# Kernel tuning notes

Hardware: AMD Instinct MI355X
Metric: run time of the kernel (lower is better)

The kernel has to match this reference:

```python
import jax, jax.numpy as jnp
import numpy as np

# Module config (matches init_kwargs)
W_BIT = 2
PS_BIT = 8
IC = 256
OC = 256
K = 3
N_XBAR = 576
STRIDE = 1
PAD = 1
NUM_IC = min(IC, N_XBAR // (K * K))   # 64 input channels per crossbar array
GROUPS = IC // NUM_IC                 # 4 arrays (col_slide), ic divides evenly
QP_W = 2 ** W_BIT - 1                 # unsigned levels for nonneg pos/neg weights
QN_PS = -(2 ** (PS_BIT - 1))          # signed psum range
QP_PS = 2 ** (PS_BIT - 1) - 1


def lsq(v, s, qn, qp):
    """LSQ quantize-dequantize with straight-through rounding."""
    vs = jnp.clip(v / s, qn, qp)
    vbar = vs + jax.lax.stop_gradient(jnp.round(vs) - vs)
    return vbar * s


def conv2d(x, w):
    # x: [B, C, H, W], w: [O, C, k, k]
    return jax.lax.conv_general_dilated(
        x, w, window_strides=(STRIDE, STRIDE),
        padding=((PAD, PAD), (PAD, PAD)),
        dimension_numbers=('NCHW', 'OIHW', 'NCHW'))


def setup_inputs() -> dict:
    key = jax.random.key(0)
    k1, k2, k3, k4, k5 = jax.random.split(key, 5)
    x = jax.random.normal(k1, (16, IC, 56, 56), dtype=jnp.float32)
    weight = jax.random.normal(k2, (OC, IC, K, K), dtype=jnp.float32) * 0.05
    # positive LSQ step sizes, roughly 2*E|w|/sqrt(Qp) scale
    w_scale = jax.random.uniform(k3, (GROUPS,), dtype=jnp.float32) * 0.04 + 0.01
    ps_scale_p = jax.random.uniform(k4, (GROUPS,), dtype=jnp.float32) * 0.05 + 0.02
    ps_scale_n = jax.random.uniform(k5, (GROUPS,), dtype=jnp.float32) * 0.05 + 0.02
    return {"x": x, "weight": weight, "w_scale": w_scale,
            "ps_scale_p": ps_scale_p, "ps_scale_n": ps_scale_n}


def reference(x, weight, w_scale, ps_scale_p, ps_scale_n):
    B, _, H, W = x.shape
    # im2col tiling over input channels into GROUPS crossbar arrays
    xg = x.reshape(B, GROUPS, NUM_IC, H, W)                  # [B,G,cg,H,W]
    wg = weight.reshape(OC, GROUPS, NUM_IC, K, K)            # [O,G,cg,k,k]
    # pos / neg weight split, per-array LSQ weight quantization (shared quantizer)
    s_w = w_scale[:, None, None, None, None]                 # [G,1,1,1,1]
    wg_t = jnp.transpose(wg, (1, 0, 2, 3, 4))                # [G,O,cg,k,k]
    wq_p = lsq(jax.nn.relu(wg_t), s_w, 0, QP_W)
    wq_n = lsq(jax.nn.relu(-wg_t), s_w, 0, QP_W)
    xg_t = jnp.transpose(xg, (1, 0, 2, 3, 4))                # [G,B,cg,H,W]
    # per-array partial-sum convs (vmapped over arrays)
    vconv = jax.vmap(conv2d, in_axes=(0, 0))
    psum_p = vconv(xg_t, wq_p)                               # [G,B,O,h,w]
    psum_n = vconv(xg_t, wq_n)
    # per-array psum LSQ quantization ('Array' mode), then accumulate
    s_p = ps_scale_p[:, None, None, None, None]
    s_n = ps_scale_n[:, None, None, None, None]
    out_p = jnp.sum(lsq(psum_p, s_p, QN_PS, QP_PS), axis=0)  # [B,O,h,w]
    out_n = jnp.sum(lsq(psum_n, s_n, QN_PS, QP_PS), axis=0)
    return out_p - out_n
```

## Files before the change

kernel.cpp:

```cpp
#include <hip/hip_runtime.h>
#include <hip/hip_bf16.h>

typedef __attribute__((ext_vector_type(8))) short bf16x8_t;
typedef __attribute__((ext_vector_type(4))) float f32x4_t;

#define XP_BYTES 55115776u
#define WT_BYTES 4718592u

typedef __attribute__((address_space(1))) const unsigned int ga_u32_t;
typedef __attribute__((address_space(3))) unsigned int lds_u32_t;

__device__ __forceinline__ void g2l16(const void* g, void* l) {
  __builtin_amdgcn_global_load_lds((ga_u32_t*)g, (lds_u32_t*)l, 16, 0, 0);
}

__global__ __launch_bounds__(256) void prep_x(const float* __restrict__ x,
                                              __hip_bfloat16* __restrict__ xp) {
  __shared__ float ls[64 * 57];
  int blk = blockIdx.x;
  int g = blk / 896;
  int r = blk - g * 896;
  int b = r / 56;
  int h = r - b * 56;
  int tid = threadIdx.x;
  const float* src = x + (size_t)(b * 256 + g * 64) * 3136 + h * 56;
  for (int i = tid; i < 64 * 56; i += 256) {
    int c = i / 56, w = i - c * 56;
    ls[c * 57 + w] = src[(size_t)c * 3136 + w];
  }
  __syncthreads();
  __hip_bfloat16* dst = xp + ((size_t)((g * 16 + b) * 58 + h + 1) * 58 + 1) * 128;
  int wp = tid >> 7;
  int inner = tid & 127;
  int hl = inner >> 6, c = inner & 63;
  for (int w0 = 0; w0 < 56; w0 += 2) {
    int w = w0 + wp;
    float v = ls[c * 57 + w];
    __hip_bfloat16 hi = __float2bfloat16(v);
    __hip_bfloat16 val = hl ? __float2bfloat16(v - __bfloat162float(hi)) : hi;
    dst[(size_t)w * 128 + inner] = val;
  }
}

__global__ __launch_bounds__(256) void prep_w(const float* __restrict__ wgt,
                                              const float* __restrict__ wsc,
                                              __hip_bfloat16* __restrict__ wt) {
  int idx = blockIdx.x * 256 + threadIdx.x;
  if (idx >= 589824) return;
  int oc = idx / 2304;
  int r = idx - oc * 2304;
  int C = r / 9;
  int tap = r - C * 9;
  int g = C >> 6, c = C & 63;
  float s = wsc[g];
  float rv = wgt[idx] / s;
  float ip = rintf(fminf(fmaxf(rv, 0.f), 3.f));
  float iN = rintf(fminf(fmaxf(-rv, 0.f), 3.f));
  size_t base_p = (size_t)(g * 512 + oc) * 1152 + tap * 128 + c;
  size_t base_n = base_p + (size_t)256 * 1152;
  __hip_bfloat16 vp = __float2bfloat16(ip);
  __hip_bfloat16 vn = __float2bfloat16(iN);
  wt[base_p] = vp;
  wt[base_p + 64] = vp;
  wt[base_n] = vn;
  wt[base_n + 64] = vn;
}

#define MEMPIN asm volatile("" ::: "memory")
#define BAR __builtin_amdgcn_s_barrier()
#define VMCNT6 asm volatile("s_waitcnt vmcnt(6)" ::: "memory")
#define VMCNT0 asm volatile("s_waitcnt vmcnt(0)" ::: "memory")

__global__ __launch_bounds__(512, 2) void conv_mfma(
    const unsigned short* __restrict__ xp, const unsigned short* __restrict__ wt,
    const float* __restrict__ wsc, const float* __restrict__ psp,
    const float* __restrict__ psn, float* __restrict__ out) {
  __shared__ char AB[3][49152];

  const int bid = blockIdx.x;
  const int wg = (bid & 7) * 49 + (bid >> 3);
  const int mblk = wg;

  const int tid = threadIdx.x;
  const int wv = tid >> 6;
  const int l = tid & 63;
  const int wr = wv >> 2, wc = wv & 3;

  const int srow = tid >> 3;
  const unsigned cs16 = (unsigned)(((tid & 7) ^ (srow & 7)) << 4);
  unsigned apix0, apix1, bofs0, bofs1, bofs2, bofs3;
  {
    int m0 = mblk * 128 + srow;
    int b0 = m0 / 3136, hw0 = m0 - b0 * 3136, h0 = hw0 / 56, w0 = hw0 - h0 * 56;
    apix0 = (unsigned)((b0 * 3364 + h0 * 58 + w0) * 256) + cs16;
    int m1 = m0 + 64;
    int b1 = m1 / 3136, hw1 = m1 - b1 * 3136, h1 = hw1 / 56, w1 = hw1 - h1 * 56;
    apix1 = (unsigned)((b1 * 3364 + h1 * 58 + w1) * 256) + cs16;
    bofs0 = (unsigned)(srow * 2304) + cs16;
    bofs1 = bofs0 + 64u * 2304u;
    bofs2 = bofs0 + 128u * 2304u;
    bofs3 = bofs0 + 192u * 2304u;
  }

  const unsigned a_base = (unsigned)((wr * 64 + (l & 15)) * 128);
  const unsigned b_base = (unsigned)(16384 + (wc * 64 + (l & 15)) * 128);
  const unsigned sw0 = (unsigned)((((l >> 4) + 0) ^ (l & 7)) << 4);
  const unsigned sw1 = (unsigned)((((l >> 4) + 4) ^ (l & 7)) << 4);

  float w0s = wsc[0], w1s = wsc[1], w2s = wsc[2], w3s = wsc[3];
  float p0 = psp[0], p1 = psp[1], p2 = psp[2], p3 = psp[3];
  float n0 = psn[0], n1 = psn[1], n2 = psn[2], n3 = psn[3];

  f32x4_t acc[4][4], oacc[4][4];
  const f32x4_t fz = {0.f, 0.f, 0.f, 0.f};
#pragma unroll
  for (int i = 0; i < 4; ++i)
#pragma unroll
    for (int j = 0; j < 4; ++j) { acc[i][j] = fz; oacc[i][j] = fz; }

  const char* xg = (const char*)xp;
  const char* wgp = (const char*)wt;

#define STAGE_A(t2)                                                            \
  {                                                                            \
    const int tt = (t2);                                                       \
    const int g_ = tt / 36;                                                    \
    const int r_ = tt - g_ * 36;                                               \
    const int s18 = (r_ >= 18) ? (r_ - 18) : r_;                               \
    const int tap_ = s18 >> 1, hl_ = s18 & 1;                                  \
    const unsigned at_ = (unsigned)g_ * 13778944u +                            \
                         (unsigned)(((tap_ / 3) * 58 + (tap_ % 3)) * 256) +    \
                         (unsigned)(hl_ << 7);                                 \
    char* lA_ = &AB[tt % 3][0] + (wv << 10);                                   \
    g2l16(xg + apix0 + at_, lA_);                                              \
    g2l16(xg + apix1 + at_, lA_ + 8192);                                       \
  }

#define STAGE_B(t2)                                                            \
  {                                                                            \
    const int tt = (t2);                                                       \
    const int g_ = tt / 36;                                                    \
    const int r_ = tt - g_ * 36;                                               \
    const int sgn_ = (r_ >= 18) ? 1 : 0;                                       \
    const int s18 = r_ - (sgn_ ? 18 : 0);                                      \
    const int tap_ = s18 >> 1, hl_ = s18 & 1;                                  \
    const unsigned bt_ = (unsigned)((g_ * 2 + sgn_) * 589824) +                \
                         (unsigned)((tap_ * 2 + hl_) << 7);                    \
    char* lB_ = &AB[tt % 3][16384] + (wv << 10);                               \
    g2l16(wgp + bofs0 + bt_, lB_);                                             \
    g2l16(wgp + bofs1 + bt_, lB_ + 8192);                                      \
    g2l16(wgp + bofs2 + bt_, lB_ + 16384);                                     \
    g2l16(wgp + bofs3 + bt_, lB_ + 24576);                                     \
  }

#define PHASE_MMA                                                              \
  __builtin_amdgcn_s_setprio(1);                                               \
  _Pragma("unroll") for (int mi = 0; mi < 4; ++mi)                             \
      _Pragma("unroll") for (int ni = 0; ni < 4; ++ni)                         \
          acc[mi][ni] = __builtin_amdgcn_mfma_f32_16x16x32_bf16(               \
              af[mi], bf[ni], acc[mi][ni], 0, 0, 0);                           \
  __builtin_amdgcn_s_setprio(0);

  STAGE_A(0); STAGE_B(0); STAGE_A(1); STAGE_B(1);

  for (int t = 0; t < 144; ++t) {
    if (t == 143) { VMCNT0; } else { VMCNT6; }
    BAR;
    MEMPIN;
    const char* buf = &AB[t % 3][0];
    bf16x8_t af[4], bf[4];
#pragma unroll
    for (int mi = 0; mi < 4; ++mi)
      af[mi] = *(const bf16x8_t*)(buf + a_base + mi * 2048 + sw0);
#pragma unroll
    for (int ni = 0; ni < 4; ++ni)
      bf[ni] = *(const bf16x8_t*)(buf + b_base + ni * 2048 + sw0);
    MEMPIN;
    if (t + 2 < 144) { STAGE_A(t + 2); }
    PHASE_MMA;
#pragma unroll
    for (int mi = 0; mi < 4; ++mi)
      af[mi] = *(const bf16x8_t*)(buf + a_base + mi * 2048 + sw1);
#pragma unroll
    for (int ni = 0; ni < 4; ++ni)
      bf[ni] = *(const bf16x8_t*)(buf + b_base + ni * 2048 + sw1);
    MEMPIN;
    if (t + 2 < 144) { STAGE_B(t + 2); }
    PHASE_MMA;

    if ((t % 18) == 17) {
      int gg = t / 36;
      int sgn = (t / 18) & 1;
      float sw = (gg & 2) ? ((gg & 1) ? w3s : w2s) : ((gg & 1) ? w1s : w0s);
      float sp = (gg & 2) ? ((gg & 1) ? p3 : p2) : ((gg & 1) ? p1 : p0);
      float sn = (gg & 2) ? ((gg & 1) ? n3 : n2) : ((gg & 1) ? n1 : n0);
      float sq = sgn ? sn : sp;
      float rs = sw / sq;
      float sgnmul = sgn ? -1.f : 1.f;
#pragma unroll
      for (int mi = 0; mi < 4; ++mi)
#pragma unroll
        for (int ni = 0; ni < 4; ++ni)
#pragma unroll
          for (int j = 0; j < 4; ++j) {
            float v = acc[mi][ni][j] * rs;
            v = fminf(fmaxf(v, -128.f), 127.f);
            oacc[mi][ni][j] += sgnmul * rintf(v) * sq;
            acc[mi][ni][j] = 0.f;
          }
    }
  }

#pragma unroll
  for (int ni = 0; ni < 4; ++ni) {
    int oc = wc * 64 + ni * 16 + (l & 15);
#pragma unroll
    for (int mi = 0; mi < 4; ++mi) {
      int m0 = mblk * 128 + wr * 64 + mi * 16 + ((l >> 4) << 2);
#pragma unroll
      for (int j = 0; j < 4; ++j) {
        int m = m0 + j;
        int b = m / 3136;
        int hw = m - b * 3136;
        out[(size_t)((b << 8) + oc) * 3136 + hw] = oacc[mi][ni][j];
      }
    }
  }
#undef STAGE_A
#undef STAGE_B
#undef PHASE_MMA
}

__global__ __launch_bounds__(256) void naive_conv(
    const float* __restrict__ x, const float* __restrict__ wgt,
    const float* __restrict__ wsc, const float* __restrict__ psp,
    const float* __restrict__ psn, float* __restrict__ out) {
  int idx = blockIdx.x * 256 + threadIdx.x;
  if (idx >= 12845056) return;
  int b = idx / 802816;
  int r = idx - b * 802816;
  int oc = r / 3136;
  int hw = r - oc * 3136;
  int h = hw / 56, w = hw - (hw / 56) * 56;
  float o = 0.f;
  for (int g = 0; g < 4; ++g) {
    float sw = wsc[g];
    float inv = 1.f / sw;
    float pp = 0.f, pn = 0.f;
    for (int tap = 0; tap < 9; ++tap) {
      int y = h + tap / 3 - 1, xx = w + tap % 3 - 1;
      if (y < 0 || y > 55 || xx < 0 || xx > 55) continue;
      const float* xr = x + (size_t)(b * 256 + g * 64) * 3136 + y * 56 + xx;
      const float* wrr = wgt + (size_t)oc * 2304 + (size_t)(g * 64) * 9 + tap;
      for (int c = 0; c < 64; ++c) {
        float xv = xr[(size_t)c * 3136];
        float rv = wrr[c * 9] * inv;
        pp += xv * rintf(fminf(fmaxf(rv, 0.f), 3.f));
        pn += xv * rintf(fminf(fmaxf(-rv, 0.f), 3.f));
      }
    }
    float sp = psp[g], sn = psn[g];
    o += rintf(fminf(fmaxf(pp * (sw / sp), -128.f), 127.f)) * sp;
    o -= rintf(fminf(fmaxf(pn * (sw / sn), -128.f), 127.f)) * sn;
  }
  out[idx] = o;
}

extern "C" void kernel_launch(void* const* d_in, const int* in_sizes, int n_in,
                              void* d_out, int out_size, void* d_ws, size_t ws_size,
                              hipStream_t stream) {
  const float* x = (const float*)d_in[0];
  const float* wgt = (const float*)d_in[1];
  const float* wsc = (const float*)d_in[2];
  const float* psp = (const float*)d_in[3];
  const float* psn = (const float*)d_in[4];
  float* out = (float*)d_out;

  if (ws_size >= (size_t)XP_BYTES + (size_t)WT_BYTES) {
    unsigned short* xpw = (unsigned short*)d_ws;
    unsigned short* wtw = (unsigned short*)((char*)d_ws + XP_BYTES);
    hipMemsetAsync(d_ws, 0, XP_BYTES, stream);
    prep_x<<<3584, 256, 0, stream>>>(x, (__hip_bfloat16*)xpw);
    prep_w<<<2304, 256, 0, stream>>>(wgt, wsc, (__hip_bfloat16*)wtw);
    conv_mfma<<<392, 512, 0, stream>>>(xpw, wtw, wsc, psp, psn, out);
  } else {
    naive_conv<<<(12845056 + 255) / 256, 256, 0, stream>>>(x, wgt, wsc, psp, psn, out);
  }
}
```

Before: 293.1 us.

## Stage one input row strip per group in LDS and reuse it across all taps

The A operand is no longer restaged from global memory for every tap. Each block now covers output rows of a single image and loads the padded input strip for a whole channel group (rows plus halo) into LDS once. All nine taps then index it with shifted pixel offsets. The weight layout drops the duplicated channel halves, so each step streams a 32-channel weight tile. This cuts global and L2 traffic for activations. In exchange, the bulk strip load at each group boundary is not overlapped with compute, and the larger LDS footprint likely limits the kernel to one block per CU.

```diff
diff --git a/kernel.cpp b/kernel.cpp
--- a/kernel.cpp
+++ b/kernel.cpp
@@ -5,7 +5,7 @@
 typedef __attribute__((ext_vector_type(4))) float f32x4_t;
 
 #define XP_BYTES 55115776u
-#define WT_BYTES 4718592u
+#define WT_BYTES 2359296u
 
 typedef __attribute__((address_space(1))) const unsigned int ga_u32_t;
 typedef __attribute__((address_space(3))) unsigned int lds_u32_t;
@@ -56,56 +56,49 @@
   float rv = wgt[idx] / s;
   float ip = rintf(fminf(fmaxf(rv, 0.f), 3.f));
   float iN = rintf(fminf(fmaxf(-rv, 0.f), 3.f));
-  size_t base_p = (size_t)(g * 512 + oc) * 1152 + tap * 128 + c;
-  size_t base_n = base_p + (size_t)256 * 1152;
-  __hip_bfloat16 vp = __float2bfloat16(ip);
-  __hip_bfloat16 vn = __float2bfloat16(iN);
-  wt[base_p] = vp;
-  wt[base_p + 64] = vp;
-  wt[base_n] = vn;
-  wt[base_n + 64] = vn;
+  size_t base_p = (size_t)((g * 2 + 0) * 256 + oc) * 576 + tap * 64 + c;
+  size_t base_n = (size_t)((g * 2 + 1) * 256 + oc) * 576 + tap * 64 + c;
+  wt[base_p] = __float2bfloat16(ip);
+  wt[base_n] = __float2bfloat16(iN);
 }
 
 #define MEMPIN asm volatile("" ::: "memory")
 #define BAR __builtin_amdgcn_s_barrier()
-#define VMCNT6 asm volatile("s_waitcnt vmcnt(6)" ::: "memory")
+#define VMCNT2 asm volatile("s_waitcnt vmcnt(2)" ::: "memory")
 #define VMCNT0 asm volatile("s_waitcnt vmcnt(0)" ::: "memory")
 
 __global__ __launch_bounds__(512, 2) void conv_mfma(
     const unsigned short* __restrict__ xp, const unsigned short* __restrict__ wt,
     const float* __restrict__ wsc, const float* __restrict__ psp,
     const float* __restrict__ psn, float* __restrict__ out) {
-  __shared__ char AB[3][49152];
+  __shared__ char Astrip[89088];
+  __shared__ char Bbuf[3][16384];
 
   const int bid = blockIdx.x;
-  const int wg = (bid & 7) * 49 + (bid >> 3);
-  const int mblk = wg;
+  const int wg = (bid & 7) * 50 + (bid >> 3);
+  const int b = wg / 25;
+  const int tile = wg - b * 25;
+  int r0 = (tile * 128) / 56; if (r0 > 52) r0 = 52;
 
   const int tid = threadIdx.x;
   const int wv = tid >> 6;
   const int l = tid & 63;
   const int wr = wv >> 2, wc = wv & 3;
 
-  const int srow = tid >> 3;
-  const unsigned cs16 = (unsigned)(((tid & 7) ^ (srow & 7)) << 4);
-  unsigned apix0, apix1, bofs0, bofs1, bofs2, bofs3;
-  {
-    int m0 = mblk * 128 + srow;
-    int b0 = m0 / 3136, hw0 = m0 - b0 * 3136, h0 = hw0 / 56, w0 = hw0 - h0 * 56;
-    apix0 = (unsigned)((b0 * 3364 + h0 * 58 + w0) * 256) + cs16;
-    int m1 = m0 + 64;
-    int b1 = m1 / 3136, hw1 = m1 - b1 * 3136, h1 = hw1 / 56, w1 = hw1 - h1 * 56;
-    apix1 = (unsigned)((b1 * 3364 + h1 * 58 + w1) * 256) + cs16;
-    bofs0 = (unsigned)(srow * 2304) + cs16;
-    bofs1 = bofs0 + 64u * 2304u;
-    bofs2 = bofs0 + 128u * 2304u;
-    bofs3 = bofs0 + 192u * 2304u;
-  }
-
-  const unsigned a_base = (unsigned)((wr * 64 + (l & 15)) * 128);
-  const unsigned b_base = (unsigned)(16384 + (wc * 64 + (l & 15)) * 128);
-  const unsigned sw0 = (unsigned)((((l >> 4) + 0) ^ (l & 7)) << 4);
-  const unsigned sw1 = (unsigned)((((l >> 4) + 4) ^ (l & 7)) << 4);
+  int pxb[4];
+#pragma unroll
+  for (int mi = 0; mi < 4; ++mi) {
+    int m = tile * 128 + wr * 64 + mi * 16 + (l & 15);
+    if (m > 3135) m = 3135;
+    int rv = m / 56, w = m - rv * 56;
+    pxb[mi] = (rv - r0) * 58 + w;
+  }
+  int boffr[4];
+#pragma unroll
+  for (int ni = 0; ni < 4; ++ni) {
+    int row = wc * 64 + ni * 16 + (l & 15);
+    boffr[ni] = row * 64 + ((((l >> 4) ^ (row & 3))) << 4);
+  }
 
   float w0s = wsc[0], w1s = wsc[1], w2s = wsc[2], w3s = wsc[3];
   float p0 = psp[0], p1 = psp[1], p2 = psp[2], p3 = psp[3];
@@ -120,83 +113,89 @@
 
   const char* xg = (const char*)xp;
   const char* wgp = (const char*)wt;
-
-#define STAGE_A(t2)                                                            \
+  const unsigned a_src = (unsigned)((b * 58 + r0) * 58) * 256u;
+
+#define STAGE_A(gg)                                                            \
   {                                                                            \
-    const int tt = (t2);                                                       \
-    const int g_ = tt / 36;                                                    \
-    const int r_ = tt - g_ * 36;                                               \
-    const int s18 = (r_ >= 18) ? (r_ - 18) : r_;                               \
-    const int tap_ = s18 >> 1, hl_ = s18 & 1;                                  \
-    const unsigned at_ = (unsigned)g_ * 13778944u +                            \
-                         (unsigned)(((tap_ / 3) * 58 + (tap_ % 3)) * 256) +    \
-                         (unsigned)(hl_ << 7);                                 \
-    char* lA_ = &AB[tt % 3][0] + (wv << 10);                                   \
-    g2l16(xg + apix0 + at_, lA_);                                              \
-    g2l16(xg + apix1 + at_, lA_ + 8192);                                       \
-  }
-
-#define STAGE_B(t2)                                                            \
+    const char* s_ = xg + (unsigned)(gg)*13778944u + a_src;                    \
+    _Pragma("unroll")                                                          \
+    for (int k_ = 0; k_ < 11; ++k_) {                                          \
+      int c_ = tid + (k_ << 9);                                                \
+      if (c_ < 5568) {                                                         \
+        int px_ = c_ >> 4, ch_ = c_ & 15;                                      \
+        g2l16(s_ + px_ * 256 + ((ch_ ^ (px_ & 7)) << 4), Astrip + c_ * 16);    \
+      }                                                                        \
+    }                                                                          \
+  }
+
+#define STAGE_B(uu)                                                            \
   {                                                                            \
-    const int tt = (t2);                                                       \
-    const int g_ = tt / 36;                                                    \
-    const int r_ = tt - g_ * 36;                                               \
-    const int sgn_ = (r_ >= 18) ? 1 : 0;                                       \
-    const int s18 = r_ - (sgn_ ? 18 : 0);                                      \
-    const int tap_ = s18 >> 1, hl_ = s18 & 1;                                  \
-    const unsigned bt_ = (unsigned)((g_ * 2 + sgn_) * 589824) +                \
-                         (unsigned)((tap_ * 2 + hl_) << 7);                    \
-    char* lB_ = &AB[tt % 3][16384] + (wv << 10);                               \
-    g2l16(wgp + bofs0 + bt_, lB_);                                             \
-    g2l16(wgp + bofs1 + bt_, lB_ + 8192);                                      \
-    g2l16(wgp + bofs2 + bt_, lB_ + 16384);                                     \
-    g2l16(wgp + bofs3 + bt_, lB_ + 24576);                                     \
-  }
-
-#define PHASE_MMA                                                              \
-  __builtin_amdgcn_s_setprio(1);                                               \
-  _Pragma("unroll") for (int mi = 0; mi < 4; ++mi)                             \
-      _Pragma("unroll") for (int ni = 0; ni < 4; ++ni)                         \
-          acc[mi][ni] = __builtin_amdgcn_mfma_f32_16x16x32_bf16(               \
-              af[mi], bf[ni], acc[mi][ni], 0, 0, 0);                           \
-  __builtin_amdgcn_s_setprio(0);
-
-  STAGE_A(0); STAGE_B(0); STAGE_A(1); STAGE_B(1);
-
-  for (int t = 0; t < 144; ++t) {
-    if (t == 143) { VMCNT0; } else { VMCNT6; }
+    const int u_ = (uu);                                                       \
+    const int g_ = u_ / 36;                                                    \
+    const int r_ = u_ - g_ * 36;                                               \
+    const int sg_ = (r_ >= 18) ? 1 : 0;                                        \
+    const int r18_ = r_ - (sg_ ? 18 : 0);                                      \
+    const char* s_ = wgp + (size_t)((g_ * 2 + sg_) * 256) * 1152 +             \
+                     (r18_ >> 1) * 128 + (r18_ & 1) * 64;                      \
+    char* d_ = &Bbuf[u_ % 3][0];                                               \
+    {                                                                          \
+      int i_ = tid, row_ = i_ >> 2;                                            \
+      g2l16(s_ + row_ * 1152 + (((i_ & 3) ^ (row_ & 3)) << 4), d_ + i_ * 16);  \
+    }                                                                          \
+    {                                                                          \
+      int i_ = tid + 512, row_ = i_ >> 2;                                      \
+      g2l16(s_ + row_ * 1152 + (((i_ & 3) ^ (row_ & 3)) << 4), d_ + i_ * 16);  \
+    }                                                                          \
+  }
+
+  STAGE_A(0);
+  STAGE_B(0);
+  STAGE_B(1);
+
+  for (int u = 0; u < 144; ++u) {
+    const int g = u / 36;
+    const int r36 = u - g * 36;
+    if (r36 == 35) { VMCNT0; } else { VMCNT2; }
     BAR;
     MEMPIN;
-    const char* buf = &AB[t % 3][0];
-    bf16x8_t af[4], bf[4];
+    const int sgn = (r36 >= 18) ? 1 : 0;
+    const int r18 = r36 - (sgn ? 18 : 0);
+    const int tap = r18 >> 1, cc = r18 & 1;
+    const int tapoff = (tap / 3) * 58 + (tap - (tap / 3) * 3);
+    const char* bbuf = &Bbuf[u % 3][0];
+
+    bf16x8_t ahi[4], alo[4], bfr[4];
+    const int kb = ((l >> 4) + cc * 4) << 4;
+#pragma unroll
+    for (int mi = 0; mi < 4; ++mi) {
+      int px = pxb[mi] + tapoff;
+      int base = (px << 8) + (kb ^ ((px & 7) << 4));
+      ahi[mi] = *(const bf16x8_t*)(Astrip + base);
+      alo[mi] = *(const bf16x8_t*)(Astrip + base + 128);
+    }
+#pragma unroll
+    for (int ni = 0; ni < 4; ++ni)
+      bfr[ni] = *(const bf16x8_t*)(bbuf + boffr[ni]);
+    MEMPIN;
+    if (r36 < 34) { STAGE_B(u + 2); }
+
+    __builtin_amdgcn_s_setprio(1);
 #pragma unroll
     for (int mi = 0; mi < 4; ++mi)
-      af[mi] = *(const bf16x8_t*)(buf + a_base + mi * 2048 + sw0);
-#pragma unroll
-    for (int ni = 0; ni < 4; ++ni)
-      bf[ni] = *(const bf16x8_t*)(buf + b_base + ni * 2048 + sw0);
-    MEMPIN;
-    if (t + 2 < 144) { STAGE_A(t + 2); }
-    PHASE_MMA;
-#pragma unroll
-    for (int mi = 0; mi < 4; ++mi)
-      af[mi] = *(const bf16x8_t*)(buf + a_base + mi * 2048 + sw1);
-#pragma unroll
-    for (int ni = 0; ni < 4; ++ni)
-      bf[ni] = *(const bf16x8_t*)(buf + b_base + ni * 2048 + sw1);
-    MEMPIN;
-    if (t + 2 < 144) { STAGE_B(t + 2); }
-    PHASE_MMA;
-
-    if ((t % 18) == 17) {
-      int gg = t / 36;
-      int sgn = (t / 18) & 1;
-      float sw = (gg & 2) ? ((gg & 1) ? w3s : w2s) : ((gg & 1) ? w1s : w0s);
-      float sp = (gg & 2) ? ((gg & 1) ? p3 : p2) : ((gg & 1) ? p1 : p0);
-      float sn = (gg & 2) ? ((gg & 1) ? n3 : n2) : ((gg & 1) ? n1 : n0);
+#pragma unroll
+      for (int ni = 0; ni < 4; ++ni) {
+        acc[mi][ni] = __builtin_amdgcn_mfma_f32_16x16x32_bf16(ahi[mi], bfr[ni], acc[mi][ni], 0, 0, 0);
+        acc[mi][ni] = __builtin_amdgcn_mfma_f32_16x16x32_bf16(alo[mi], bfr[ni], acc[mi][ni], 0, 0, 0);
+      }
+    __builtin_amdgcn_s_setprio(0);
+
+    if ((u % 18) == 17) {
+      float sw = (g & 2) ? ((g & 1) ? w3s : w2s) : ((g & 1) ? w1s : w0s);
+      float sp = (g & 2) ? ((g & 1) ? p3 : p2) : ((g & 1) ? p1 : p0);
+      float sn = (g & 2) ? ((g & 1) ? n3 : n2) : ((g & 1) ? n1 : n0);
       float sq = sgn ? sn : sp;
       float rs = sw / sq;
-      float sgnmul = sgn ? -1.f : 1.f;
+      float sgnmul = sgn ? -sq : sq;
 #pragma unroll
       for (int mi = 0; mi < 4; ++mi)
 #pragma unroll
@@ -205,30 +204,35 @@
           for (int j = 0; j < 4; ++j) {
             float v = acc[mi][ni][j] * rs;
             v = fminf(fmaxf(v, -128.f), 127.f);
-            oacc[mi][ni][j] += sgnmul * rintf(v) * sq;
+            oacc[mi][ni][j] += sgnmul * rintf(v);
             acc[mi][ni][j] = 0.f;
           }
     }
+
+    if (r36 == 35 && u < 143) {
+      BAR;
+      STAGE_A(g + 1);
+      STAGE_B(u + 1);
+      STAGE_B(u + 2);
+    }
   }
 
 #pragma unroll
   for (int ni = 0; ni < 4; ++ni) {
     int oc = wc * 64 + ni * 16 + (l & 15);
+    float* orow = out + ((size_t)(b * 256 + oc)) * 3136;
 #pragma unroll
     for (int mi = 0; mi < 4; ++mi) {
-      int m0 = mblk * 128 + wr * 64 + mi * 16 + ((l >> 4) << 2);
+      int m0 = tile * 128 + wr * 64 + mi * 16 + ((l >> 4) << 2);
 #pragma unroll
       for (int j = 0; j < 4; ++j) {
         int m = m0 + j;
-        int b = m / 3136;
-        int hw = m - b * 3136;
-        out[(size_t)((b << 8) + oc) * 3136 + hw] = oacc[mi][ni][j];
+        if (m < 3136) orow[m] = oacc[mi][ni][j];
       }
     }
   }
 #undef STAGE_A
 #undef STAGE_B
-#undef PHASE_MMA
 }
 
 __global__ __launch_bounds__(256) void naive_conv(
@@ -282,7 +286,7 @@
     hipMemsetAsync(d_ws, 0, XP_BYTES, stream);
     prep_x<<<3584, 256, 0, stream>>>(x, (__hip_bfloat16*)xpw);
     prep_w<<<2304, 256, 0, stream>>>(wgt, wsc, (__hip_bfloat16*)wtw);
-    conv_mfma<<<392, 512, 0, stream>>>(xpw, wtw, wsc, psp, psn, out);
+    conv_mfma<<<400, 512, 0, stream>>>(xpw, wtw, wsc, psp, psn, out);
   } else {
     naive_conv<<<(12845056 + 255) / 256, 256, 0, stream>>>(x, wgt, wsc, psp, psn, out);
   }
```

New measurement: 356.3 us. 1.22x slower.
